# Performance work log

Measured on AMD Instinct MI355X. Metric: run time of the kernel, lower is better.

## Reference

```python
import jax, jax.numpy as jnp
import numpy as np
import math

B, IN, OUT = 1024, 512, 512


def setup_inputs() -> dict:
    key = jax.random.key(0)
    ks = jax.random.split(key, 7)
    std = 1.0 / math.sqrt(IN)
    x = jax.random.normal(ks[0], (B, IN), dtype=jnp.float32)
    base_weight = jax.random.uniform(ks[1], (OUT, IN), dtype=jnp.float32, minval=-std, maxval=std)
    chirplet_weights = jax.random.uniform(ks[2], (OUT, IN), dtype=jnp.float32, minval=-std, maxval=std)
    # scale init ones, frequency ones, translation zeros; add small jitter for a non-degenerate test point
    scale = 1.0 + 0.1 * jax.random.normal(ks[3], (OUT, IN), dtype=jnp.float32)
    translation = 0.1 * jax.random.normal(ks[4], (OUT, IN), dtype=jnp.float32)
    frequency = 1.0 + 0.1 * jax.random.normal(ks[5], (OUT, IN), dtype=jnp.float32)
    bias = jax.random.uniform(ks[6], (OUT,), dtype=jnp.float32, minval=-std, maxval=std)
    return {"x": x, "base_weight": base_weight, "chirplet_weights": chirplet_weights,
            "scale": scale, "translation": translation, "frequency": frequency, "bias": bias}


def reference(x, base_weight, chirplet_weights, scale, translation, frequency, bias):
    TWO_PI = 2.0 * math.pi
    # base linear path: SiLU(x) @ W^T
    base_out = jnp.einsum('bi,oi->bo', jax.nn.silu(x), base_weight)
    # chirplet path: (b, o, i) intermediate reduced over i
    x_scaled = (x[:, None, :] - translation[None, :, :]) / scale[None, :, :]  # (B, OUT, IN)
    chirplet = jnp.cos(TWO_PI * frequency[None, :, :] * x_scaled) * jnp.exp(-0.5 * x_scaled ** 2)
    chirplet_out = jnp.einsum('boi,oi->bo', chirplet, chirplet_weights)
    return base_out + chirplet_out + bias[None, :]
```

## Files before the change

### kernel.cpp

```cpp
#include <hip/hip_runtime.h>
#include <hip/hip_bf16.h>

#define B_ 1024
#define IN_ 512
#define OUT_ 512
#define BTILE 64
#define OTILE 16
#define ITILE 16
#define KSPLIT 8
#define KCHUNK (IN_ / KSPLIT)
#define NCHUNKS (KCHUNK / ITILE)
#define P4STRIDE 64
#define P2STRIDE 32
#define XSTRIDE 68

__device__ __forceinline__ float fast_exp2(float x) {
#if __has_builtin(__builtin_amdgcn_exp2f)
    return __builtin_amdgcn_exp2f(x);
#else
    return __exp2f(x);
#endif
}
__device__ __forceinline__ float fast_log2(float x) {
#if __has_builtin(__builtin_amdgcn_logf)
    return __builtin_amdgcn_logf(x);
#else
    return __log2f(x);
#endif
}
__device__ __forceinline__ float fast_cos_rev(float x) {
#if __has_builtin(__builtin_amdgcn_cosf)
    return __builtin_amdgcn_cosf(x);
#else
    return __cosf(x * 6.2831853071795864f);
#endif
}
__device__ __forceinline__ float fast_rcp(float x) {
#if __has_builtin(__builtin_amdgcn_rcpf)
    return __builtin_amdgcn_rcpf(x);
#else
    return 1.0f / x;
#endif
}

__global__ __launch_bounds__(256, 8) void chirplet_kernel(
    const float* __restrict__ x,
    const float* __restrict__ W,
    const float* __restrict__ Wc,
    const float* __restrict__ S,
    const float* __restrict__ T,
    const float* __restrict__ F,
    const float* __restrict__ bias,
    float* __restrict__ out)
{
    __shared__ __align__(16) float p4_lds[ITILE * P4STRIDE];
    __shared__ __align__(16) float p2_lds[ITILE * P2STRIDE];
    __shared__ __align__(16) float x_lds[ITILE * XSTRIDE];
    __shared__ __align__(16) float s_lds[ITILE * XSTRIDE];

    const int tid = threadIdx.x;
    const int o0 = blockIdx.x * OTILE;
    const int b0 = blockIdx.y * BTILE;
    const int k0 = blockIdx.z * KCHUNK;

    const int oc = tid & 15;
    const int bq = tid >> 4;

    const int xrow = tid >> 2;
    const int xq   = tid & 3;

    const int pol = tid & 15;
    const int pi  = tid >> 4;

    const float LOG2E = 1.4426950408889634f;
    const float GK    = 0.8493218002880191f;

    float acc[4] = {0.f, 0.f, 0.f, 0.f};

    for (int c = 0; c < NCHUNKS; ++c) {
        const int ib = k0 + c * ITILE;

        {
            const float4 v = *(const float4*)(x + (size_t)(b0 + xrow) * IN_ + ib + xq * 4);
            const float xf[4] = { v.x, v.y, v.z, v.w };
            #pragma unroll
            for (int j = 0; j < 4; ++j) {
                const int col = xq * 4 + j;
                float xv  = xf[j];
                float sig = fast_rcp(1.0f + fast_exp2(-xv * LOG2E));
                x_lds[col * XSTRIDE + xrow] = xv;
                s_lds[col * XSTRIDE + xrow] = xv * sig;
            }
        }

        {
            const size_t go = (size_t)(o0 + pol) * IN_ + k0 + c * ITILE + pi;
            const float s  = S[go];
            const float t  = T[go];
            const float f  = F[go];
            const float w  = W[go];
            const float wc = Wc[go];
            const float rs = fast_rcp(s);
            const float a  = f * rs;
            float4 p0; float2 p1;
            p0.x = a;
            p0.y = -a * t + (wc < 0.0f ? 0.5f : 0.0f);
            p0.z = rs * GK;
            p0.w = -t * rs * GK;
            p1.x = fast_log2(fabsf(wc));
            p1.y = w;
            *(float4*)&p4_lds[pi * P4STRIDE + pol * 4] = p0;
            *(float2*)&p2_lds[pi * P2STRIDE + pol * 2] = p1;
        }
        __syncthreads();

        #pragma unroll 4
        for (int i = 0; i < ITILE; ++i) {
            const float4 abcd = *(const float4*)&p4_lds[i * P4STRIDE + oc * 4];
            const float2 lww  = *(const float2*)&p2_lds[i * P2STRIDE + oc * 2];
            const float4 xv   = *(const float4*)&x_lds[i * XSTRIDE + bq * 4];
            const float4 svv  = *(const float4*)&s_lds[i * XSTRIDE + bq * 4];
            const float xk[4] = { xv.x, xv.y, xv.z, xv.w };
            const float sk[4] = { svv.x, svv.y, svv.z, svv.w };
            #pragma unroll
            for (int k = 0; k < 4; ++k) {
                float rev = fmaf(abcd.x, xk[k], abcd.y);
                float co  = fast_cos_rev(rev);
                float u   = fmaf(abcd.z, xk[k], abcd.w);
                float e   = fast_exp2(fmaf(-u, u, lww.x));
                acc[k] = fmaf(co, e, acc[k]);
                acc[k] = fmaf(sk[k], lww.y, acc[k]);
            }
        }
        __syncthreads();
    }

    const float badd = (blockIdx.z == 0) ? bias[o0 + oc] : 0.0f;
    #pragma unroll
    for (int k = 0; k < 4; ++k) {
        const int b = b0 + bq * 4 + k;
        float* dst = &out[(size_t)b * OUT_ + o0 + oc];
#if defined(__HIP_DEVICE_COMPILE__)
        unsafeAtomicAdd(dst, acc[k] + badd);
#else
        atomicAdd(dst, acc[k] + badd);
#endif
    }
}

extern "C" void kernel_launch(void* const* d_in, const int* in_sizes, int n_in,
                              void* d_out, int out_size, void* d_ws, size_t ws_size,
                              hipStream_t stream) {
    const float* x    = (const float*)d_in[0];
    const float* W    = (const float*)d_in[1];
    const float* Wc   = (const float*)d_in[2];
    const float* S    = (const float*)d_in[3];
    const float* T    = (const float*)d_in[4];
    const float* F    = (const float*)d_in[5];
    const float* bias = (const float*)d_in[6];
    float* out = (float*)d_out;

    hipMemsetAsync(out, 0, (size_t)out_size * sizeof(float), stream);

    dim3 grid(OUT_ / OTILE, B_ / BTILE, KSPLIT);
    chirplet_kernel<<<grid, 256, 0, stream>>>(x, W, Wc, S, T, F, bias, out);
}
```

Measured before the change: 135.1 us.

## Hold per-output chirplet parameters in registers and use packed FMA

Each thread now owns one output column and keeps the precomputed chirplet parameters for an 8-wide K chunk in registers, instead of staging them through LDS. K is split into 64 chunks across the grid and the batch loop is walked in groups of 4. Arithmetic uses packed 2-wide FMAs to cut VALU instructions, and LDS parameter traffic and the inner-loop barriers are removed. The cost is eight times more global atomic adds into the output, since every K chunk writes its own partial sums.

```diff
diff --git a/kernel.cpp b/kernel.cpp
--- a/kernel.cpp
+++ b/kernel.cpp
@@ -4,15 +4,13 @@
 #define B_ 1024
 #define IN_ 512
 #define OUT_ 512
-#define BTILE 64
-#define OTILE 16
-#define ITILE 16
-#define KSPLIT 8
-#define KCHUNK (IN_ / KSPLIT)
-#define NCHUNKS (KCHUNK / ITILE)
-#define P4STRIDE 64
-#define P2STRIDE 32
-#define XSTRIDE 68
+#define BTILE 32
+#define OTILE 256
+#define KCHUNK 8
+#define KSPLIT (IN_ / KCHUNK)
+
+typedef float v2f __attribute__((ext_vector_type(2)));
+#define PKFMA(a, b, c) __builtin_elementwise_fma((v2f)(a), (v2f)(b), (v2f)(c))
 
 __device__ __forceinline__ float fast_exp2(float x) {
 #if __has_builtin(__builtin_amdgcn_exp2f)
@@ -43,7 +41,7 @@
 #endif
 }
 
-__global__ __launch_bounds__(256, 8) void chirplet_kernel(
+__global__ __launch_bounds__(256, 6) void chirplet_kernel(
     const float* __restrict__ x,
     const float* __restrict__ W,
     const float* __restrict__ Wc,
@@ -53,98 +51,91 @@
     const float* __restrict__ bias,
     float* __restrict__ out)
 {
-    __shared__ __align__(16) float p4_lds[ITILE * P4STRIDE];
-    __shared__ __align__(16) float p2_lds[ITILE * P2STRIDE];
-    __shared__ __align__(16) float x_lds[ITILE * XSTRIDE];
-    __shared__ __align__(16) float s_lds[ITILE * XSTRIDE];
+    __shared__ __align__(16) float x_lds[KCHUNK * BTILE];
+    __shared__ __align__(16) float s_lds[KCHUNK * BTILE];
 
     const int tid = threadIdx.x;
-    const int o0 = blockIdx.x * OTILE;
+    const int o  = blockIdx.x * OTILE + tid;
     const int b0 = blockIdx.y * BTILE;
-    const int k0 = blockIdx.z * KCHUNK;
-
-    const int oc = tid & 15;
-    const int bq = tid >> 4;
-
-    const int xrow = tid >> 2;
-    const int xq   = tid & 3;
-
-    const int pol = tid & 15;
-    const int pi  = tid >> 4;
+    const int ib = blockIdx.z * KCHUNK;
 
     const float LOG2E = 1.4426950408889634f;
     const float GK    = 0.8493218002880191f;
 
-    float acc[4] = {0.f, 0.f, 0.f, 0.f};
-
-    for (int c = 0; c < NCHUNKS; ++c) {
-        const int ib = k0 + c * ITILE;
-
-        {
-            const float4 v = *(const float4*)(x + (size_t)(b0 + xrow) * IN_ + ib + xq * 4);
-            const float xf[4] = { v.x, v.y, v.z, v.w };
-            #pragma unroll
-            for (int j = 0; j < 4; ++j) {
-                const int col = xq * 4 + j;
-                float xv  = xf[j];
-                float sig = fast_rcp(1.0f + fast_exp2(-xv * LOG2E));
-                x_lds[col * XSTRIDE + xrow] = xv;
-                s_lds[col * XSTRIDE + xrow] = xv * sig;
-            }
-        }
-
-        {
-            const size_t go = (size_t)(o0 + pol) * IN_ + k0 + c * ITILE + pi;
-            const float s  = S[go];
-            const float t  = T[go];
-            const float f  = F[go];
-            const float w  = W[go];
-            const float wc = Wc[go];
-            const float rs = fast_rcp(s);
-            const float a  = f * rs;
-            float4 p0; float2 p1;
-            p0.x = a;
-            p0.y = -a * t + (wc < 0.0f ? 0.5f : 0.0f);
-            p0.z = rs * GK;
-            p0.w = -t * rs * GK;
-            p1.x = fast_log2(fabsf(wc));
-            p1.y = w;
-            *(float4*)&p4_lds[pi * P4STRIDE + pol * 4] = p0;
-            *(float2*)&p2_lds[pi * P2STRIDE + pol * 2] = p1;
-        }
-        __syncthreads();
-
-        #pragma unroll 4
-        for (int i = 0; i < ITILE; ++i) {
-            const float4 abcd = *(const float4*)&p4_lds[i * P4STRIDE + oc * 4];
-            const float2 lww  = *(const float2*)&p2_lds[i * P2STRIDE + oc * 2];
-            const float4 xv   = *(const float4*)&x_lds[i * XSTRIDE + bq * 4];
-            const float4 svv  = *(const float4*)&s_lds[i * XSTRIDE + bq * 4];
-            const float xk[4] = { xv.x, xv.y, xv.z, xv.w };
-            const float sk[4] = { svv.x, svv.y, svv.z, svv.w };
-            #pragma unroll
-            for (int k = 0; k < 4; ++k) {
-                float rev = fmaf(abcd.x, xk[k], abcd.y);
-                float co  = fast_cos_rev(rev);
-                float u   = fmaf(abcd.z, xk[k], abcd.w);
-                float e   = fast_exp2(fmaf(-u, u, lww.x));
-                acc[k] = fmaf(co, e, acc[k]);
-                acc[k] = fmaf(sk[k], lww.y, acc[k]);
-            }
-        }
-        __syncthreads();
+    {
+        const int sb = tid >> 3;
+        const int si = tid & 7;
+        const float xv  = x[(size_t)(b0 + sb) * IN_ + ib + si];
+        const float sig = fast_rcp(1.0f + fast_exp2(-xv * LOG2E));
+        x_lds[si * BTILE + sb] = xv;
+        s_lds[si * BTILE + sb] = xv * sig;
     }
 
-    const float badd = (blockIdx.z == 0) ? bias[o0 + oc] : 0.0f;
-    #pragma unroll
-    for (int k = 0; k < 4; ++k) {
-        const int b = b0 + bq * 4 + k;
-        float* dst = &out[(size_t)b * OUT_ + o0 + oc];
+    float pa[KCHUNK], pb[KCHUNK], pc[KCHUNK], pd[KCHUNK], plw[KCHUNK], pw[KCHUNK];
+    {
+        const size_t ro = (size_t)o * IN_ + ib;
+        const float4 sA = *(const float4*)(S  + ro), sB = *(const float4*)(S  + ro + 4);
+        const float4 tA = *(const float4*)(T  + ro), tB = *(const float4*)(T  + ro + 4);
+        const float4 fA = *(const float4*)(F  + ro), fB = *(const float4*)(F  + ro + 4);
+        const float4 wA = *(const float4*)(W  + ro), wB = *(const float4*)(W  + ro + 4);
+        const float4 cA = *(const float4*)(Wc + ro), cB = *(const float4*)(Wc + ro + 4);
+        const float sv[8] = { sA.x,sA.y,sA.z,sA.w, sB.x,sB.y,sB.z,sB.w };
+        const float tv[8] = { tA.x,tA.y,tA.z,tA.w, tB.x,tB.y,tB.z,tB.w };
+        const float fv[8] = { fA.x,fA.y,fA.z,fA.w, fB.x,fB.y,fB.z,fB.w };
+        const float wv[8] = { wA.x,wA.y,wA.z,wA.w, wB.x,wB.y,wB.z,wB.w };
+        const float cv[8] = { cA.x,cA.y,cA.z,cA.w, cB.x,cB.y,cB.z,cB.w };
+        #pragma unroll
+        for (int i = 0; i < KCHUNK; ++i) {
+            const float rs = fast_rcp(sv[i]);
+            const float a  = fv[i] * rs;
+            pa[i]  = a;
+            pb[i]  = -a * tv[i] + (cv[i] < 0.0f ? 0.5f : 0.0f);
+            pc[i]  = rs * GK;
+            pd[i]  = -tv[i] * rs * GK;
+            plw[i] = fast_log2(fabsf(cv[i]));
+            pw[i]  = wv[i];
+        }
+    }
+    __syncthreads();
+
+    const float badd = (blockIdx.z == 0) ? bias[o] : 0.0f;
+
+    for (int bq = 0; bq < BTILE / 4; ++bq) {
+        v2f acc01 = {0.f, 0.f}, acc23 = {0.f, 0.f};
+        #pragma unroll
+        for (int i = 0; i < KCHUNK; ++i) {
+            const float4 xv = *(const float4*)&x_lds[i * BTILE + bq * 4];
+            const float4 sl = *(const float4*)&s_lds[i * BTILE + bq * 4];
+            const v2f x01 = { xv.x, xv.y }, x23 = { xv.z, xv.w };
+            const v2f s01 = { sl.x, sl.y }, s23 = { sl.z, sl.w };
+            const v2f A  = { pa[i],  pa[i]  };
+            const v2f Bv = { pb[i],  pb[i]  };
+            const v2f C  = { pc[i],  pc[i]  };
+            const v2f D  = { pd[i],  pd[i]  };
+            const v2f LW = { plw[i], plw[i] };
+            const v2f Wv = { pw[i],  pw[i]  };
+
+            v2f rev01 = PKFMA(A, x01, Bv), rev23 = PKFMA(A, x23, Bv);
+            v2f u01   = PKFMA(C, x01, D),  u23   = PKFMA(C, x23, D);
+            v2f g01   = PKFMA(-u01, u01, LW), g23 = PKFMA(-u23, u23, LW);
+            v2f co01, co23, e01, e23;
+            co01.x = fast_cos_rev(rev01.x);  co01.y = fast_cos_rev(rev01.y);
+            co23.x = fast_cos_rev(rev23.x);  co23.y = fast_cos_rev(rev23.y);
+            e01.x  = fast_exp2(g01.x);       e01.y  = fast_exp2(g01.y);
+            e23.x  = fast_exp2(g23.x);       e23.y  = fast_exp2(g23.y);
+            acc01 = PKFMA(co01, e01, acc01); acc23 = PKFMA(co23, e23, acc23);
+            acc01 = PKFMA(s01, Wv, acc01);   acc23 = PKFMA(s23, Wv, acc23);
+        }
+        const float vals[4] = { acc01.x, acc01.y, acc23.x, acc23.y };
+        #pragma unroll
+        for (int j = 0; j < 4; ++j) {
+            float* dst = &out[(size_t)(b0 + bq * 4 + j) * OUT_ + o];
 #if defined(__HIP_DEVICE_COMPILE__)
-        unsafeAtomicAdd(dst, acc[k] + badd);
+            unsafeAtomicAdd(dst, vals[j] + badd);
 #else
-        atomicAdd(dst, acc[k] + badd);
+            atomicAdd(dst, vals[j] + badd);
 #endif
+        }
     }
 }
 
```

Measured after the change: 298.9 us. 121% more time.
